# Optimization experiments

Measured on AMD Instinct MI355X. Metric: run time of the kernel, lower is better.

## Reference

```python
import jax, jax.numpy as jnp
import numpy as np
import math

N_POINTS = 1_000_000
DIM = 3
N_LEVELS = 16
N_FEATS = 2
LOG2_HASHMAP = 19
BASE_RES = 16
DESIRED_RES = 2048
HASH_PRIMES = np.array([1, 2654435761, 805459861], dtype=np.uint32)


def _level_params():
    # faithful to original: denominator is (base_resolution - 1)
    beta = math.exp((math.log(DESIRED_RES) - math.log(BASE_RES)) / (BASE_RES - 1))
    res, hs = [], []
    for l in range(N_LEVELS):
        r = math.floor(BASE_RES * beta ** l)
        res.append(float(r))
        hs.append(min(r ** DIM, 2 ** LOG2_HASHMAP))
    return np.array(res, np.float32), np.array(hs, np.uint32)


def setup_inputs() -> dict:
    key = jax.random.key(0)
    k1, k2 = jax.random.split(key)
    x = jax.random.uniform(k1, (N_POINTS, DIM), dtype=jnp.float32)
    tables = jax.random.uniform(k2, (N_LEVELS, 2 ** LOG2_HASHMAP, N_FEATS),
                                dtype=jnp.float32, minval=-1e-4, maxval=1e-4)
    return {"x": x, "tables": tables}


def reference(x, tables):
    res_np, hs_np = _level_params()
    resolutions = jnp.asarray(res_np)           # [L]
    hashmap_sizes = jnp.asarray(hs_np)          # [L] uint32
    primes = jnp.asarray(HASH_PRIMES)           # [3] uint32
    neigs = np.arange(1 << DIM, dtype=np.int64).reshape(-1, 1)
    dims = np.arange(DIM, dtype=np.int64).reshape(1, -1)
    bin_mask = jnp.asarray((neigs & (1 << dims)) == 0)  # [8,3] bool

    def level(table, resolution, hashmap_size):
        xs = x * resolution                      # [N,3]
        xi = xs.astype(jnp.int32)                # trunc (x >= 0 so == floor)
        xf = xs - xi.astype(xs.dtype)
        xi = xi[:, None, :]                      # [N,1,3]
        xf = xf[:, None, :]
        inds = jnp.where(bin_mask, xi, xi + 1)   # [N,8,3]
        ws = jnp.where(bin_mask, 1.0 - xf, xf)   # [N,8,3]
        w = jnp.prod(ws, axis=-1, keepdims=True) # [N,8,1]
        # hash: 32-bit prime multiply, xor fold, mod hashmap_size
        h = inds.astype(jnp.uint32) * primes     # [N,8,3] (wraps mod 2^32)
        h = h[..., 0] ^ h[..., 1] ^ h[..., 2]    # [N,8]
        hid = (h % hashmap_size).astype(jnp.int32)
        return jnp.sum(table[hid] * w, axis=-2)  # [N,F]

    feats = jax.vmap(level)(tables, resolutions, hashmap_sizes)  # [L,N,F]
    feats = jnp.moveaxis(feats, 0, 1).reshape(x.shape[0], N_LEVELS * N_FEATS)
    # include_input=True
    return jnp.concatenate([x, feats], axis=-1)  # [N, 3 + L*F]
```

## Files before the change

### kernel.cpp

```cpp
#include <hip/hip_runtime.h>
#include <cstdint>
#include <cstddef>


#define NPTS     1000000
#define NLEV     16
#define TBL_ENT  524288
#define BLK      256
#define OUT_PP   35
#define CHUNKS   ((NPTS + BLK - 1) / BLK)

typedef float f32x2 __attribute__((ext_vector_type(2)));

constexpr float    cRes[NLEV] = {16.f, 22.f, 30.f, 42.f, 58.f, 80.f, 111.f, 153.f,
                                 212.f, 294.f, 406.f, 561.f, 776.f, 1072.f, 1482.f, 2048.f};
constexpr uint32_t cHS[NLEV]  = {4096u, 10648u, 27000u, 74088u, 195112u, 512000u,
                                 524288u, 524288u, 524288u, 524288u, 524288u,
                                 524288u, 524288u, 524288u, 524288u, 524288u};


template<int L>
__device__ __forceinline__ void do_level(float px, float py, float pz,
                                         const float* __restrict__ tables,
                                         float& f0, float& f1)
{
    constexpr float    r  = cRes[L];
    constexpr uint32_t hs = cHS[L];
    const float2* __restrict__ tbl =
        reinterpret_cast<const float2*>(tables) + (size_t)L * TBL_ENT;

    const float xs = px * r, ys = py * r, zs = pz * r;
    const int xi = (int)xs, yi = (int)ys, zi = (int)zs;
    const float xf = xs - (float)xi, yf = ys - (float)yi, zf = zs - (float)zi;

    const uint32_t hx0 = (uint32_t)xi;
    const uint32_t hx1 = hx0 + 1u;
    const uint32_t hy0 = (uint32_t)yi * 2654435761u;
    const uint32_t hy1 = hy0 + 2654435761u;
    const uint32_t hz0 = (uint32_t)zi * 805459861u;
    const uint32_t hz1 = hz0 + 805459861u;

    const float wx0 = 1.f - xf, wx1 = xf;
    const float wy0 = 1.f - yf, wy1 = yf;
    const float wz0 = 1.f - zf, wz1 = zf;

    uint32_t hid[8];
    float    w[8];
    #pragma unroll
    for (int c = 0; c < 8; ++c) {
        const uint32_t hxc = (c & 1) ? hx1 : hx0;
        const uint32_t hyc = (c & 2) ? hy1 : hy0;
        const uint32_t hzc = (c & 4) ? hz1 : hz0;
        hid[c] = (hxc ^ hyc ^ hzc) % hs;
        const float wxc = (c & 1) ? wx1 : wx0;
        const float wyc = (c & 2) ? wy1 : wy0;
        const float wzc = (c & 4) ? wz1 : wz0;
        w[c] = wxc * wyc * wzc;
    }

    float2 v[8];
    #pragma unroll
    for (int c = 0; c < 8; ++c) v[c] = tbl[hid[c]];

    f0 = 0.f; f1 = 0.f;
    #pragma unroll
    for (int c = 0; c < 8; ++c) {
        f0 = fmaf(w[c], v[c].x, f0);
        f1 = fmaf(w[c], v[c].y, f1);
    }
}


__global__ __launch_bounds__(BLK) void hashgrid_pass1(
    const float* __restrict__ x,
    const float* __restrict__ tables,
    float2* __restrict__ ws)
{
    const int b = blockIdx.x;
    const int l = b / CHUNKS;
    const int c = b - l * CHUNKS;
    const int i = c * BLK + threadIdx.x;
    if (i >= NPTS) return;

    const float px = __builtin_nontemporal_load(&x[3 * i + 0]);
    const float py = __builtin_nontemporal_load(&x[3 * i + 1]);
    const float pz = __builtin_nontemporal_load(&x[3 * i + 2]);

    float f0, f1;
    switch (l) {
        case 0:  do_level<0 >(px, py, pz, tables, f0, f1); break;
        case 1:  do_level<1 >(px, py, pz, tables, f0, f1); break;
        case 2:  do_level<2 >(px, py, pz, tables, f0, f1); break;
        case 3:  do_level<3 >(px, py, pz, tables, f0, f1); break;
        case 4:  do_level<4 >(px, py, pz, tables, f0, f1); break;
        case 5:  do_level<5 >(px, py, pz, tables, f0, f1); break;
        case 6:  do_level<6 >(px, py, pz, tables, f0, f1); break;
        case 7:  do_level<7 >(px, py, pz, tables, f0, f1); break;
        case 8:  do_level<8 >(px, py, pz, tables, f0, f1); break;
        case 9:  do_level<9 >(px, py, pz, tables, f0, f1); break;
        case 10: do_level<10>(px, py, pz, tables, f0, f1); break;
        case 11: do_level<11>(px, py, pz, tables, f0, f1); break;
        case 12: do_level<12>(px, py, pz, tables, f0, f1); break;
        case 13: do_level<13>(px, py, pz, tables, f0, f1); break;
        case 14: do_level<14>(px, py, pz, tables, f0, f1); break;
        default: do_level<15>(px, py, pz, tables, f0, f1); break;
    }

    f32x2 o; o.x = f0; o.y = f1;
    __builtin_nontemporal_store(o,
        reinterpret_cast<f32x2*>(ws) + (size_t)l * NPTS + i);
}


__global__ __launch_bounds__(BLK) void hashgrid_pass2(
    const float* __restrict__ x,
    const float2* __restrict__ ws,
    float* __restrict__ out)
{
    __shared__ float smem[BLK * OUT_PP];

    const int t = threadIdx.x;
    const int base = blockIdx.x * BLK;
    const int i = base + t;
    const bool active = (i < NPTS);

    if (active) {
        smem[t * OUT_PP + 0] = x[3 * i + 0];
        smem[t * OUT_PP + 1] = x[3 * i + 1];
        smem[t * OUT_PP + 2] = x[3 * i + 2];
        #pragma unroll
        for (int l = 0; l < NLEV; ++l) {
            const float2 v = ws[(size_t)l * NPTS + i];
            smem[t * OUT_PP + 3 + 2 * l]     = v.x;
            smem[t * OUT_PP + 3 + 2 * l + 1] = v.y;
        }
    }
    __syncthreads();

    const size_t gbase = (size_t)blockIdx.x * (BLK * OUT_PP);
    const long long remain = (long long)NPTS * OUT_PP - (long long)gbase;
    const int n4 = (int)((remain < (long long)(BLK * OUT_PP) ? remain : (long long)(BLK * OUT_PP)) / 4);
    const float4* __restrict__ s4 = reinterpret_cast<const float4*>(smem);
    float4* __restrict__ o4 = reinterpret_cast<float4*>(out + gbase);
    for (int j = t; j < n4; j += BLK) o4[j] = s4[j];
}


__global__ __launch_bounds__(BLK) void hashgrid_fused(
    const float* __restrict__ x,
    const float* __restrict__ tables,
    float* __restrict__ out)
{
    __shared__ float smem[BLK * OUT_PP];

    const int t = threadIdx.x;
    const int i = blockIdx.x * BLK + t;
    const bool active = (i < NPTS);

    float px = 0.f, py = 0.f, pz = 0.f;
    if (active) {
        px = x[3 * i + 0];
        py = x[3 * i + 1];
        pz = x[3 * i + 2];
    }
    smem[t * OUT_PP + 0] = px;
    smem[t * OUT_PP + 1] = py;
    smem[t * OUT_PP + 2] = pz;

    float f0, f1;
    #pragma unroll
    for (int l = 0; l < NLEV; ++l) {
        switch (l) {
            case 0:  do_level<0 >(px, py, pz, tables, f0, f1); break;
            case 1:  do_level<1 >(px, py, pz, tables, f0, f1); break;
            case 2:  do_level<2 >(px, py, pz, tables, f0, f1); break;
            case 3:  do_level<3 >(px, py, pz, tables, f0, f1); break;
            case 4:  do_level<4 >(px, py, pz, tables, f0, f1); break;
            case 5:  do_level<5 >(px, py, pz, tables, f0, f1); break;
            case 6:  do_level<6 >(px, py, pz, tables, f0, f1); break;
            case 7:  do_level<7 >(px, py, pz, tables, f0, f1); break;
            case 8:  do_level<8 >(px, py, pz, tables, f0, f1); break;
            case 9:  do_level<9 >(px, py, pz, tables, f0, f1); break;
            case 10: do_level<10>(px, py, pz, tables, f0, f1); break;
            case 11: do_level<11>(px, py, pz, tables, f0, f1); break;
            case 12: do_level<12>(px, py, pz, tables, f0, f1); break;
            case 13: do_level<13>(px, py, pz, tables, f0, f1); break;
            case 14: do_level<14>(px, py, pz, tables, f0, f1); break;
            default: do_level<15>(px, py, pz, tables, f0, f1); break;
        }
        smem[t * OUT_PP + 3 + 2 * l]     = f0;
        smem[t * OUT_PP + 3 + 2 * l + 1] = f1;
    }

    __syncthreads();

    const size_t gbase = (size_t)blockIdx.x * (BLK * OUT_PP);
    const long long remain = (long long)NPTS * OUT_PP - (long long)gbase;
    const int n4 = (int)((remain < (long long)(BLK * OUT_PP) ? remain : (long long)(BLK * OUT_PP)) / 4);
    const float4* __restrict__ s4 = reinterpret_cast<const float4*>(smem);
    float4* __restrict__ o4 = reinterpret_cast<float4*>(out + gbase);
    for (int j = t; j < n4; j += BLK) o4[j] = s4[j];
}

extern "C" void kernel_launch(void* const* d_in, const int* in_sizes, int n_in,
                              void* d_out, int out_size, void* d_ws, size_t ws_size,
                              hipStream_t stream)
{
    const float* x      = (const float*)d_in[0];
    const float* tables = (const float*)d_in[1];
    float* out          = (float*)d_out;

    const size_t ws_needed = (size_t)NLEV * NPTS * sizeof(float2);

    if (ws_size >= ws_needed) {
        float2* ws = (float2*)d_ws;
        hashgrid_pass1<<<NLEV * CHUNKS, BLK, 0, stream>>>(x, tables, ws);
        hashgrid_pass2<<<CHUNKS, BLK, 0, stream>>>(x, ws, out);
    } else {
        hashgrid_fused<<<CHUNKS, BLK, 0, stream>>>(x, tables, out);
    }
}
```

Measured before the change: 552.1 us.

## Write per-level features directly to output, dropping workspace transpose pass

```diff
diff --git a/kernel.cpp b/kernel.cpp
--- a/kernel.cpp
+++ b/kernel.cpp
@@ -9,8 +9,6 @@
 #define BLK      256
 #define OUT_PP   35
 #define CHUNKS   ((NPTS + BLK - 1) / BLK)
-
-typedef float f32x2 __attribute__((ext_vector_type(2)));
 
 constexpr float    cRes[NLEV] = {16.f, 22.f, 30.f, 42.f, 58.f, 80.f, 111.f, 153.f,
                                  212.f, 294.f, 406.f, 561.f, 776.f, 1072.f, 1482.f, 2048.f};
@@ -71,10 +69,10 @@
 }
 
 
-__global__ __launch_bounds__(BLK) void hashgrid_pass1(
+__global__ __launch_bounds__(BLK) void hashgrid_direct(
     const float* __restrict__ x,
     const float* __restrict__ tables,
-    float2* __restrict__ ws)
+    float* __restrict__ out)
 {
     const int b = blockIdx.x;
     const int l = b / CHUNKS;
@@ -106,43 +104,14 @@
         default: do_level<15>(px, py, pz, tables, f0, f1); break;
     }
 
-    f32x2 o; o.x = f0; o.y = f1;
-    __builtin_nontemporal_store(o,
-        reinterpret_cast<f32x2*>(ws) + (size_t)l * NPTS + i);
-}
-
-
-__global__ __launch_bounds__(BLK) void hashgrid_pass2(
-    const float* __restrict__ x,
-    const float2* __restrict__ ws,
-    float* __restrict__ out)
-{
-    __shared__ float smem[BLK * OUT_PP];
-
-    const int t = threadIdx.x;
-    const int base = blockIdx.x * BLK;
-    const int i = base + t;
-    const bool active = (i < NPTS);
-
-    if (active) {
-        smem[t * OUT_PP + 0] = x[3 * i + 0];
-        smem[t * OUT_PP + 1] = x[3 * i + 1];
-        smem[t * OUT_PP + 2] = x[3 * i + 2];
-        #pragma unroll
-        for (int l = 0; l < NLEV; ++l) {
-            const float2 v = ws[(size_t)l * NPTS + i];
-            smem[t * OUT_PP + 3 + 2 * l]     = v.x;
-            smem[t * OUT_PP + 3 + 2 * l + 1] = v.y;
-        }
+    float* __restrict__ o = out + (size_t)i * OUT_PP;
+    o[3 + 2 * l]  = f0;
+    o[4 + 2 * l]  = f1;
+    if (l == 0) {
+        o[0] = px;
+        o[1] = py;
+        o[2] = pz;
     }
-    __syncthreads();
-
-    const size_t gbase = (size_t)blockIdx.x * (BLK * OUT_PP);
-    const long long remain = (long long)NPTS * OUT_PP - (long long)gbase;
-    const int n4 = (int)((remain < (long long)(BLK * OUT_PP) ? remain : (long long)(BLK * OUT_PP)) / 4);
-    const float4* __restrict__ s4 = reinterpret_cast<const float4*>(smem);
-    float4* __restrict__ o4 = reinterpret_cast<float4*>(out + gbase);
-    for (int j = t; j < n4; j += BLK) o4[j] = s4[j];
 }
 
 
@@ -210,13 +179,6 @@
     const float* tables = (const float*)d_in[1];
     float* out          = (float*)d_out;
 
-    const size_t ws_needed = (size_t)NLEV * NPTS * sizeof(float2);
-
-    if (ws_size >= ws_needed) {
-        float2* ws = (float2*)d_ws;
-        hashgrid_pass1<<<NLEV * CHUNKS, BLK, 0, stream>>>(x, tables, ws);
-        hashgrid_pass2<<<CHUNKS, BLK, 0, stream>>>(x, ws, out);
-    } else {
-        hashgrid_fused<<<CHUNKS, BLK, 0, stream>>>(x, tables, out);
-    }
+    hashgrid_direct<<<NLEV * CHUNKS, BLK, 0, stream>>>(x, tables, out);
+    (void)d_ws; (void)ws_size;
 }
```

After: 739.6 us. 34.0% more time.

## Software-pipeline pass2 over multiple tiles per block and use plain ws stores

Applied to the files above, without the earlier changes.

```diff
diff --git a/kernel.cpp b/kernel.cpp
--- a/kernel.cpp
+++ b/kernel.cpp
@@ -9,8 +9,8 @@
 #define BLK      256
 #define OUT_PP   35
 #define CHUNKS   ((NPTS + BLK - 1) / BLK)
-
-typedef float f32x2 __attribute__((ext_vector_type(2)));
+#define P2_TPB   4
+#define P2GRID   ((CHUNKS + P2_TPB - 1) / P2_TPB)
 
 constexpr float    cRes[NLEV] = {16.f, 22.f, 30.f, 42.f, 58.f, 80.f, 111.f, 153.f,
                                  212.f, 294.f, 406.f, 561.f, 776.f, 1072.f, 1482.f, 2048.f};
@@ -106,11 +106,26 @@
         default: do_level<15>(px, py, pz, tables, f0, f1); break;
     }
 
-    f32x2 o; o.x = f0; o.y = f1;
-    __builtin_nontemporal_store(o,
-        reinterpret_cast<f32x2*>(ws) + (size_t)l * NPTS + i);
-}
-
+    ws[(size_t)l * NPTS + i] = make_float2(f0, f1);
+}
+
+
+__device__ __forceinline__ void load_row(const float* __restrict__ x,
+                                         const float2* __restrict__ ws,
+                                         int i, bool act, float (&r)[OUT_PP])
+{
+    if (act) {
+        r[0] = x[3 * i + 0];
+        r[1] = x[3 * i + 1];
+        r[2] = x[3 * i + 2];
+        #pragma unroll
+        for (int l = 0; l < NLEV; ++l) {
+            const float2 v = ws[(size_t)l * NPTS + i];
+            r[3 + 2 * l]     = v.x;
+            r[4 + 2 * l]     = v.y;
+        }
+    }
+}
 
 __global__ __launch_bounds__(BLK) void hashgrid_pass2(
     const float* __restrict__ x,
@@ -120,29 +135,49 @@
     __shared__ float smem[BLK * OUT_PP];
 
     const int t = threadIdx.x;
-    const int base = blockIdx.x * BLK;
-    const int i = base + t;
-    const bool active = (i < NPTS);
-
-    if (active) {
-        smem[t * OUT_PP + 0] = x[3 * i + 0];
-        smem[t * OUT_PP + 1] = x[3 * i + 1];
-        smem[t * OUT_PP + 2] = x[3 * i + 2];
+    const int tile0 = blockIdx.x * P2_TPB;
+
+    float cur[OUT_PP], nxt[OUT_PP];
+
+    {
+        const int i = tile0 * BLK + t;
+        load_row(x, ws, i, (tile0 < CHUNKS) && (i < NPTS), cur);
+    }
+
+    #pragma unroll
+    for (int k = 0; k < P2_TPB; ++k) {
+        const int tile = tile0 + k;
+        if (tile >= CHUNKS) break;
+
+        {
+            const int ntile = tile + 1;
+            const bool hasN = (k + 1 < P2_TPB) && (ntile < CHUNKS);
+            const int i = ntile * BLK + t;
+            load_row(x, ws, i, hasN && (i < NPTS), nxt);
+        }
+
+        {
+            const int i = tile * BLK + t;
+            if (i < NPTS) {
+                #pragma unroll
+                for (int q = 0; q < OUT_PP; ++q) smem[t * OUT_PP + q] = cur[q];
+            }
+        }
+        __syncthreads();
+
+        {
+            const size_t gbase = (size_t)tile * (BLK * OUT_PP);
+            const long long remain = (long long)NPTS * OUT_PP - (long long)gbase;
+            const int n4 = (int)((remain < (long long)(BLK * OUT_PP) ? remain : (long long)(BLK * OUT_PP)) / 4);
+            const float4* __restrict__ s4 = reinterpret_cast<const float4*>(smem);
+            float4* __restrict__ o4 = reinterpret_cast<float4*>(out + gbase);
+            for (int j = t; j < n4; j += BLK) o4[j] = s4[j];
+        }
+        __syncthreads();
+
         #pragma unroll
-        for (int l = 0; l < NLEV; ++l) {
-            const float2 v = ws[(size_t)l * NPTS + i];
-            smem[t * OUT_PP + 3 + 2 * l]     = v.x;
-            smem[t * OUT_PP + 3 + 2 * l + 1] = v.y;
-        }
-    }
-    __syncthreads();
-
-    const size_t gbase = (size_t)blockIdx.x * (BLK * OUT_PP);
-    const long long remain = (long long)NPTS * OUT_PP - (long long)gbase;
-    const int n4 = (int)((remain < (long long)(BLK * OUT_PP) ? remain : (long long)(BLK * OUT_PP)) / 4);
-    const float4* __restrict__ s4 = reinterpret_cast<const float4*>(smem);
-    float4* __restrict__ o4 = reinterpret_cast<float4*>(out + gbase);
-    for (int j = t; j < n4; j += BLK) o4[j] = s4[j];
+        for (int q = 0; q < OUT_PP; ++q) cur[q] = nxt[q];
+    }
 }
 
 
@@ -215,7 +250,7 @@
     if (ws_size >= ws_needed) {
         float2* ws = (float2*)d_ws;
         hashgrid_pass1<<<NLEV * CHUNKS, BLK, 0, stream>>>(x, tables, ws);
-        hashgrid_pass2<<<CHUNKS, BLK, 0, stream>>>(x, ws, out);
+        hashgrid_pass2<<<P2GRID, BLK, 0, stream>>>(x, ws, out);
     } else {
         hashgrid_fused<<<CHUNKS, BLK, 0, stream>>>(x, tables, out);
     }
```

Result: no change. 552.2 us (+0.0%).

## Store hash tables and per-level intermediates in scaled fp16

Applied to the files above, without the earlier changes.

```diff
diff --git a/kernel.cpp b/kernel.cpp
--- a/kernel.cpp
+++ b/kernel.cpp
@@ -9,8 +9,10 @@
 #define BLK      256
 #define OUT_PP   35
 #define CHUNKS   ((NPTS + BLK - 1) / BLK)
-
-typedef float f32x2 __attribute__((ext_vector_type(2)));
+#define NENT     (NLEV * TBL_ENT)
+
+#define SCALE     8192.0f
+#define INV_SCALE (1.0f / 8192.0f)
 
 constexpr float    cRes[NLEV] = {16.f, 22.f, 30.f, 42.f, 58.f, 80.f, 111.f, 153.f,
                                  212.f, 294.f, 406.f, 561.f, 776.f, 1072.f, 1482.f, 2048.f};
@@ -18,16 +20,31 @@
                                  524288u, 524288u, 524288u, 524288u, 524288u,
                                  524288u, 524288u, 524288u, 524288u, 524288u};
 
+union H2 { uint32_t u; _Float16 h[2]; };
+
+
+__global__ __launch_bounds__(BLK) void cvt_tables(
+    const float2* __restrict__ tin,
+    uint32_t* __restrict__ tout)
+{
+    const int e = blockIdx.x * BLK + threadIdx.x;
+    if (e >= NENT) return;
+    const float2 v = tin[e];
+    H2 p;
+    p.h[0] = (_Float16)(v.x * SCALE);
+    p.h[1] = (_Float16)(v.y * SCALE);
+    tout[e] = p.u;
+}
+
 
 template<int L>
-__device__ __forceinline__ void do_level(float px, float py, float pz,
-                                         const float* __restrict__ tables,
-                                         float& f0, float& f1)
+__device__ __forceinline__ void do_level16(float px, float py, float pz,
+                                           const uint32_t* __restrict__ tbl16,
+                                           float& f0, float& f1)
 {
     constexpr float    r  = cRes[L];
     constexpr uint32_t hs = cHS[L];
-    const float2* __restrict__ tbl =
-        reinterpret_cast<const float2*>(tables) + (size_t)L * TBL_ENT;
+    const uint32_t* __restrict__ tbl = tbl16 + (size_t)L * TBL_ENT;
 
     const float xs = px * r, ys = py * r, zs = pz * r;
     const int xi = (int)xs, yi = (int)ys, zi = (int)zs;
@@ -58,6 +75,58 @@
         w[c] = wxc * wyc * wzc;
     }
 
+    uint32_t raw[8];
+    #pragma unroll
+    for (int c = 0; c < 8; ++c) raw[c] = tbl[hid[c]];
+
+    f0 = 0.f; f1 = 0.f;
+    #pragma unroll
+    for (int c = 0; c < 8; ++c) {
+        H2 p; p.u = raw[c];
+        f0 = fmaf(w[c], (float)p.h[0], f0);
+        f1 = fmaf(w[c], (float)p.h[1], f1);
+    }
+}
+
+template<int L>
+__device__ __forceinline__ void do_level_f32(float px, float py, float pz,
+                                             const float* __restrict__ tables,
+                                             float& f0, float& f1)
+{
+    constexpr float    r  = cRes[L];
+    constexpr uint32_t hs = cHS[L];
+    const float2* __restrict__ tbl =
+        reinterpret_cast<const float2*>(tables) + (size_t)L * TBL_ENT;
+
+    const float xs = px * r, ys = py * r, zs = pz * r;
+    const int xi = (int)xs, yi = (int)ys, zi = (int)zs;
+    const float xf = xs - (float)xi, yf = ys - (float)yi, zf = zs - (float)zi;
+
+    const uint32_t hx0 = (uint32_t)xi;
+    const uint32_t hx1 = hx0 + 1u;
+    const uint32_t hy0 = (uint32_t)yi * 2654435761u;
+    const uint32_t hy1 = hy0 + 2654435761u;
+    const uint32_t hz0 = (uint32_t)zi * 805459861u;
+    const uint32_t hz1 = hz0 + 805459861u;
+
+    const float wx0 = 1.f - xf, wx1 = xf;
+    const float wy0 = 1.f - yf, wy1 = yf;
+    const float wz0 = 1.f - zf, wz1 = zf;
+
+    uint32_t hid[8];
+    float    w[8];
+    #pragma unroll
+    for (int c = 0; c < 8; ++c) {
+        const uint32_t hxc = (c & 1) ? hx1 : hx0;
+        const uint32_t hyc = (c & 2) ? hy1 : hy0;
+        const uint32_t hzc = (c & 4) ? hz1 : hz0;
+        hid[c] = (hxc ^ hyc ^ hzc) % hs;
+        const float wxc = (c & 1) ? wx1 : wx0;
+        const float wyc = (c & 2) ? wy1 : wy0;
+        const float wzc = (c & 4) ? wz1 : wz0;
+        w[c] = wxc * wyc * wzc;
+    }
+
     float2 v[8];
     #pragma unroll
     for (int c = 0; c < 8; ++c) v[c] = tbl[hid[c]];
@@ -73,8 +142,8 @@
 
 __global__ __launch_bounds__(BLK) void hashgrid_pass1(
     const float* __restrict__ x,
-    const float* __restrict__ tables,
-    float2* __restrict__ ws)
+    const uint32_t* __restrict__ tbl16,
+    uint32_t* __restrict__ wsF)
 {
     const int b = blockIdx.x;
     const int l = b / CHUNKS;
@@ -88,40 +157,40 @@
 
     float f0, f1;
     switch (l) {
-        case 0:  do_level<0 >(px, py, pz, tables, f0, f1); break;
-        case 1:  do_level<1 >(px, py, pz, tables, f0, f1); break;
-        case 2:  do_level<2 >(px, py, pz, tables, f0, f1); break;
-        case 3:  do_level<3 >(px, py, pz, tables, f0, f1); break;
-        case 4:  do_level<4 >(px, py, pz, tables, f0, f1); break;
-        case 5:  do_level<5 >(px, py, pz, tables, f0, f1); break;
-        case 6:  do_level<6 >(px, py, pz, tables, f0, f1); break;
-        case 7:  do_level<7 >(px, py, pz, tables, f0, f1); break;
-        case 8:  do_level<8 >(px, py, pz, tables, f0, f1); break;
-        case 9:  do_level<9 >(px, py, pz, tables, f0, f1); break;
-        case 10: do_level<10>(px, py, pz, tables, f0, f1); break;
-        case 11: do_level<11>(px, py, pz, tables, f0, f1); break;
-        case 12: do_level<12>(px, py, pz, tables, f0, f1); break;
-        case 13: do_level<13>(px, py, pz, tables, f0, f1); break;
-        case 14: do_level<14>(px, py, pz, tables, f0, f1); break;
-        default: do_level<15>(px, py, pz, tables, f0, f1); break;
-    }
-
-    f32x2 o; o.x = f0; o.y = f1;
-    __builtin_nontemporal_store(o,
-        reinterpret_cast<f32x2*>(ws) + (size_t)l * NPTS + i);
+        case 0:  do_level16<0 >(px, py, pz, tbl16, f0, f1); break;
+        case 1:  do_level16<1 >(px, py, pz, tbl16, f0, f1); break;
+        case 2:  do_level16<2 >(px, py, pz, tbl16, f0, f1); break;
+        case 3:  do_level16<3 >(px, py, pz, tbl16, f0, f1); break;
+        case 4:  do_level16<4 >(px, py, pz, tbl16, f0, f1); break;
+        case 5:  do_level16<5 >(px, py, pz, tbl16, f0, f1); break;
+        case 6:  do_level16<6 >(px, py, pz, tbl16, f0, f1); break;
+        case 7:  do_level16<7 >(px, py, pz, tbl16, f0, f1); break;
+        case 8:  do_level16<8 >(px, py, pz, tbl16, f0, f1); break;
+        case 9:  do_level16<9 >(px, py, pz, tbl16, f0, f1); break;
+        case 10: do_level16<10>(px, py, pz, tbl16, f0, f1); break;
+        case 11: do_level16<11>(px, py, pz, tbl16, f0, f1); break;
+        case 12: do_level16<12>(px, py, pz, tbl16, f0, f1); break;
+        case 13: do_level16<13>(px, py, pz, tbl16, f0, f1); break;
+        case 14: do_level16<14>(px, py, pz, tbl16, f0, f1); break;
+        default: do_level16<15>(px, py, pz, tbl16, f0, f1); break;
+    }
+
+    H2 o;
+    o.h[0] = (_Float16)f0;
+    o.h[1] = (_Float16)f1;
+    wsF[(size_t)l * NPTS + i] = o.u;
 }
 
 
 __global__ __launch_bounds__(BLK) void hashgrid_pass2(
     const float* __restrict__ x,
-    const float2* __restrict__ ws,
+    const uint32_t* __restrict__ wsF,
     float* __restrict__ out)
 {
     __shared__ float smem[BLK * OUT_PP];
 
     const int t = threadIdx.x;
-    const int base = blockIdx.x * BLK;
-    const int i = base + t;
+    const int i = blockIdx.x * BLK + t;
     const bool active = (i < NPTS);
 
     if (active) {
@@ -130,9 +199,9 @@
         smem[t * OUT_PP + 2] = x[3 * i + 2];
         #pragma unroll
         for (int l = 0; l < NLEV; ++l) {
-            const float2 v = ws[(size_t)l * NPTS + i];
-            smem[t * OUT_PP + 3 + 2 * l]     = v.x;
-            smem[t * OUT_PP + 3 + 2 * l + 1] = v.y;
+            H2 p; p.u = wsF[(size_t)l * NPTS + i];
+            smem[t * OUT_PP + 3 + 2 * l]     = (float)p.h[0] * INV_SCALE;
+            smem[t * OUT_PP + 3 + 2 * l + 1] = (float)p.h[1] * INV_SCALE;
         }
     }
     __syncthreads();
@@ -171,22 +240,22 @@
     #pragma unroll
     for (int l = 0; l < NLEV; ++l) {
         switch (l) {
-            case 0:  do_level<0 >(px, py, pz, tables, f0, f1); break;
-            case 1:  do_level<1 >(px, py, pz, tables, f0, f1); break;
-            case 2:  do_level<2 >(px, py, pz, tables, f0, f1); break;
-            case 3:  do_level<3 >(px, py, pz, tables, f0, f1); break;
-            case 4:  do_level<4 >(px, py, pz, tables, f0, f1); break;
-            case 5:  do_level<5 >(px, py, pz, tables, f0, f1); break;
-            case 6:  do_level<6 >(px, py, pz, tables, f0, f1); break;
-            case 7:  do_level<7 >(px, py, pz, tables, f0, f1); break;
-            case 8:  do_level<8 >(px, py, pz, tables, f0, f1); break;
-            case 9:  do_level<9 >(px, py, pz, tables, f0, f1); break;
-            case 10: do_level<10>(px, py, pz, tables, f0, f1); break;
-            case 11: do_level<11>(px, py, pz, tables, f0, f1); break;
-            case 12: do_level<12>(px, py, pz, tables, f0, f1); break;
-            case 13: do_level<13>(px, py, pz, tables, f0, f1); break;
-            case 14: do_level<14>(px, py, pz, tables, f0, f1); break;
-            default: do_level<15>(px, py, pz, tables, f0, f1); break;
+            case 0:  do_level_f32<0 >(px, py, pz, tables, f0, f1); break;
+            case 1:  do_level_f32<1 >(px, py, pz, tables, f0, f1); break;
+            case 2:  do_level_f32<2 >(px, py, pz, tables, f0, f1); break;
+            case 3:  do_level_f32<3 >(px, py, pz, tables, f0, f1); break;
+            case 4:  do_level_f32<4 >(px, py, pz, tables, f0, f1); break;
+            case 5:  do_level_f32<5 >(px, py, pz, tables, f0, f1); break;
+            case 6:  do_level_f32<6 >(px, py, pz, tables, f0, f1); break;
+            case 7:  do_level_f32<7 >(px, py, pz, tables, f0, f1); break;
+            case 8:  do_level_f32<8 >(px, py, pz, tables, f0, f1); break;
+            case 9:  do_level_f32<9 >(px, py, pz, tables, f0, f1); break;
+            case 10: do_level_f32<10>(px, py, pz, tables, f0, f1); break;
+            case 11: do_level_f32<11>(px, py, pz, tables, f0, f1); break;
+            case 12: do_level_f32<12>(px, py, pz, tables, f0, f1); break;
+            case 13: do_level_f32<13>(px, py, pz, tables, f0, f1); break;
+            case 14: do_level_f32<14>(px, py, pz, tables, f0, f1); break;
+            default: do_level_f32<15>(px, py, pz, tables, f0, f1); break;
         }
         smem[t * OUT_PP + 3 + 2 * l]     = f0;
         smem[t * OUT_PP + 3 + 2 * l + 1] = f1;
@@ -210,12 +279,15 @@
     const float* tables = (const float*)d_in[1];
     float* out          = (float*)d_out;
 
-    const size_t ws_needed = (size_t)NLEV * NPTS * sizeof(float2);
+    const size_t ws_needed = (size_t)NENT * 4 + (size_t)NLEV * NPTS * 4;
 
     if (ws_size >= ws_needed) {
-        float2* ws = (float2*)d_ws;
-        hashgrid_pass1<<<NLEV * CHUNKS, BLK, 0, stream>>>(x, tables, ws);
-        hashgrid_pass2<<<CHUNKS, BLK, 0, stream>>>(x, ws, out);
+        uint32_t* tbl16 = (uint32_t*)d_ws;
+        uint32_t* wsF   = tbl16 + NENT;
+        cvt_tables<<<(NENT + BLK - 1) / BLK, BLK, 0, stream>>>(
+            (const float2*)tables, tbl16);
+        hashgrid_pass1<<<NLEV * CHUNKS, BLK, 0, stream>>>(x, tbl16, wsF);
+        hashgrid_pass2<<<CHUNKS, BLK, 0, stream>>>(x, wsF, out);
     } else {
         hashgrid_fused<<<CHUNKS, BLK, 0, stream>>>(x, tables, out);
     }
```

Measured after the change: 563.8 us. 1.02x slower.
